# Performance work log

Hardware: AMD Instinct MI355X
Metric: run time of the kernel (lower is better)

## Reference

```python
import jax, jax.numpy as jnp
import numpy as np

B, N = 2, 2048
DIM, NH, DH = 640, 10, 64
DINNER = 2560
L = 4
DEMB = 32
NTOKS = [128, 64]
NFEAT = 19
FDIM = 280
FEATD = DIM - DEMB * len(NTOKS)  # 576
SQRTD = float(np.sqrt(DH))


def _ln(x, g, b, eps=1e-5):
    m = jnp.mean(x, -1, keepdims=True)
    v = jnp.var(x, -1, keepdims=True)
    return (x - m) * jax.lax.rsqrt(v + eps) * g + b


def setup_inputs() -> dict:
    key = jax.random.key(0)
    ks = iter(jax.random.split(key, 32))
    s = 0.05
    return {
        "x_feats": jax.random.normal(next(ks), (B, N, NFEAT), jnp.float32),
        "x_toks": jax.random.randint(next(ks), (B, N, 2), 0, 64),
        "mask": jnp.ones((B, N), jnp.float32),
        "emb0": jax.random.normal(next(ks), (NTOKS[0] + 1, DEMB)) * s,
        "emb1": jax.random.normal(next(ks), (NTOKS[1] + 1, DEMB)) * s,
        "feat_w": jax.random.normal(next(ks), (FEATD, NFEAT)) * s,
        "feat_b": jnp.zeros((FEATD,)),
        "qkv_w": jax.random.normal(next(ks), (L, 3 * DIM, DIM)) * s,
        "qkv_b": jnp.zeros((L, 3 * DIM)),
        "o_w": jax.random.normal(next(ks), (L, DIM, DIM)) * s,
        "ln1_g": jnp.ones((L, DIM)), "ln1_b": jnp.zeros((L, DIM)),
        "ln2_g": jnp.ones((L, DIM)), "ln2_b": jnp.zeros((L, DIM)),
        "p1_w": jax.random.normal(next(ks), (L, DINNER, DIM)) * s,
        "p1_b": jnp.zeros((L, DINNER)),
        "p2_w": jax.random.normal(next(ks), (L, DIM, DINNER)) * s,
        "p2_b": jnp.zeros((L, DIM)),
        "fn_g": jnp.ones((DIM,)), "fn_b": jnp.zeros((DIM,)),
        "lin1_w": jax.random.normal(next(ks), (FDIM, DIM)) * s,
        "lin1_b": jnp.zeros((FDIM,)),
        "rb1_w": jax.random.normal(next(ks), (FDIM, FDIM)) * s,
        "rb1_b": jnp.zeros((FDIM,)),
        "rb2_w": jax.random.normal(next(ks), (FDIM, FDIM)) * s,
        "rb2_b": jnp.zeros((FDIM,)),
        "out_w": jax.random.normal(next(ks), (1, FDIM)) * s,
        "out_b": jnp.zeros((1,)),
    }


def _forward(x_feats, x_toks, mask, emb0, emb1, feat_w, feat_b,
             qkv_w, qkv_b, o_w, ln1_g, ln1_b, ln2_g, ln2_b,
             p1_w, p1_b, p2_w, p2_b, fn_g, fn_b,
             lin1_w, lin1_b, rb1_w, rb1_b, rb2_w, rb2_b, out_w, out_b):
    # mask outer product [B,N,N]; additive mask 0 where allowed, -1e20 elsewhere
    mask2 = jnp.einsum('bi,bj->bij', mask, mask)
    add_mask = jnp.where(mask2 > 0, 0.0, -1e20)

    # embeddings + feature projection -> [B,N,DIM]
    Z = jnp.concatenate([emb0[x_toks[..., 0]], emb1[x_toks[..., 1]],
                         x_feats @ feat_w.T + feat_b], axis=-1)

    def layer(Z, prm):
        qw, qb, ow, g1, b1, g2, b2, w1, c1, w2, c2 = prm
        inp = Z
        Zn = _ln(Z, g1, b1)
        # qkv reshaped to [B,N,H,3*DH], chunked along last dim: V, Q, K
        qkv = (Zn @ qw.T + qb).reshape(B, N, NH, 3 * DH)
        V, Q, K = qkv[..., :DH], qkv[..., DH:2 * DH], qkv[..., 2 * DH:]
        W = jnp.einsum('bnhd,bmhd->bhnm', Q, K) / SQRTD + add_mask[:, None]
        W = jax.nn.softmax(W, axis=3) * mask2[:, None]  # post-softmax mult mask
        attn = jnp.einsum('bhnm,bmhd->bnhd', W, V).reshape(B, N, DIM)
        Z = jax.nn.leaky_relu(attn) @ ow.T + inp  # leaky_relu BEFORE o_net
        inp = Z
        Zn = _ln(Z, g2, b2)
        Z = jax.nn.relu(Zn @ w1.T + c1) @ w2.T + c2 + inp
        return Z, None

    Z, _ = jax.lax.scan(layer, Z,
                        (qkv_w, qkv_b, o_w, ln1_g, ln1_b, ln2_g, ln2_b,
                         p1_w, p1_b, p2_w, p2_b))
    Z = _ln(Z, fn_g, fn_b)
    # ranking head: 1x1 convs == per-token linears
    h = Z @ lin1_w.T + lin1_b
    h = h + (jax.nn.relu(h @ rb1_w.T + rb1_b) @ rb2_w.T + rb2_b)
    return (h @ out_w.T + out_b)[..., 0]  # [B,N]


def reference(x_feats, x_toks, mask, emb0, emb1, feat_w, feat_b,
              qkv_w, qkv_b, o_w, ln1_g, ln1_b, ln2_g, ln2_b,
              p1_w, p1_b, p2_w, p2_b, fn_g, fn_b,
              lin1_w, lin1_b, rb1_w, rb1_b, rb2_w, rb2_b, out_w, out_b):
    return _forward(x_feats, x_toks, mask, emb0, emb1, feat_w, feat_b,
                    qkv_w, qkv_b, o_w, ln1_g, ln1_b, ln2_g, ln2_b,
                    p1_w, p1_b, p2_w, p2_b, fn_g, fn_b,
                    lin1_w, lin1_b, rb1_w, rb1_b, rb2_w, rb2_b, out_w, out_b)
```

## Files before the change

### kernel.cpp

```cpp
#include <hip/hip_runtime.h>

#define B_ 2
#define N_ 2048
#define DIM_ 640
#define NH_ 10
#define DH_ 64
#define DINNER_ 2560
#define L_ 4
#define FDIM_ 280
#define FDIMP_ 320
#define FEATD_ 576
#define NFEAT_ 19
#define ROWS_ (B_*N_)

typedef __attribute__((ext_vector_type(8))) unsigned short ushort8;
typedef __attribute__((ext_vector_type(8))) __bf16 bf16x8;
typedef __attribute__((ext_vector_type(4))) __bf16 bf16x4;
typedef __attribute__((ext_vector_type(4))) float f32x4;
typedef __attribute__((ext_vector_type(2))) unsigned int u32x2;

static __device__ __forceinline__ unsigned short f2bf(float f){
  unsigned int u = __builtin_bit_cast(unsigned int, f);
  u += 0x7fffu + ((u >> 16) & 1u);
  return (unsigned short)(u >> 16);
}

static __device__ __forceinline__ f32x4 mfma16(ushort8 a, ushort8 b, f32x4 c){
  return __builtin_amdgcn_mfma_f32_16x16x32_bf16(
      __builtin_bit_cast(bf16x8, a), __builtin_bit_cast(bf16x8, b), c, 0, 0, 0);
}

#define GLD(src,dst) __builtin_amdgcn_global_load_lds((const __attribute__((address_space(1))) void*)(src), (__attribute__((address_space(3))) void*)(dst), 16, 0, 0)

#define SEG0 4915200
#define SEG1 1638400
#define SEG2 6553600
#define SEG3 6553600
#define SEG4 179200
#define SEG5 89600
#define SEG6 89600
#define SEG7 655360
#define SEG8 655360
#define SEG9 4096
#define E0 SEG0
#define E1 (E0+SEG1)
#define E2 (E1+SEG2)
#define E3 (E2+SEG3)
#define E4 (E3+SEG4)
#define E5 (E4+SEG5)
#define E6 (E5+SEG6)
#define E7 (E6+SEG7)
#define E8 (E7+SEG8)
#define E9 (E8+SEG9)

__global__ __launch_bounds__(256) void prep_kernel(
    const float* __restrict__ qkv_w, const float* __restrict__ o_w,
    const float* __restrict__ p1_w, const float* __restrict__ p2_w,
    const float* __restrict__ lin1_w, const float* __restrict__ rb1_w,
    const float* __restrict__ rb2_w, const float* __restrict__ mask,
    unsigned short* __restrict__ qkvw, unsigned short* __restrict__ oww,
    unsigned short* __restrict__ p1w, unsigned short* __restrict__ p2w,
    unsigned short* __restrict__ l1w, unsigned short* __restrict__ r1w,
    unsigned short* __restrict__ r2w, unsigned int* __restrict__ hb1z,
    unsigned int* __restrict__ hb2z, float* __restrict__ mbb)
{
  for (int i = blockIdx.x*256 + threadIdx.x; i < E9; i += gridDim.x*256){
    int j = i;
    if (j < E0) { qkvw[j] = f2bf(qkv_w[j]); continue; }
    j -= E0;
    if (j < SEG1) { oww[j] = f2bf(o_w[j]); continue; }
    j -= SEG1;
    if (j < SEG2) { p1w[j] = f2bf(p1_w[j]); continue; }
    j -= SEG2;
    if (j < SEG3) { p2w[j] = f2bf(p2_w[j]); continue; }
    j -= SEG3;
    if (j < SEG4) { l1w[j] = f2bf(lin1_w[j]); continue; }
    j -= SEG4;
    if (j < SEG5) { int r = j/FDIMP_, c = j - r*FDIMP_;
                    r1w[j] = (c<FDIM_) ? f2bf(rb1_w[r*FDIM_+c]) : (unsigned short)0; continue; }
    j -= SEG5;
    if (j < SEG6) { int r = j/FDIMP_, c = j - r*FDIMP_;
                    r2w[j] = (c<FDIM_) ? f2bf(rb2_w[r*FDIM_+c]) : (unsigned short)0; continue; }
    j -= SEG6;
    if (j < SEG7) { hb1z[j] = 0u; continue; }
    j -= SEG7;
    if (j < SEG8) { hb2z[j] = 0u; continue; }
    j -= SEG8;
    mbb[j] = (mask[j] > 0.f) ? 0.f : -1e30f;
  }
}

__global__ __launch_bounds__(256) void embed_kernel(const float* __restrict__ xf,
    const int* __restrict__ xt, const float* __restrict__ e0, const float* __restrict__ e1,
    const float* __restrict__ fw, const float* __restrict__ fb, float* __restrict__ Z){
  int row = blockIdx.x;
  __shared__ float f[NFEAT_];
  int t = threadIdx.x;
  if (t < NFEAT_) f[t] = xf[row*NFEAT_ + t];
  __syncthreads();
  if (t < 32) {
    int tok0 = xt[row*2];
    Z[(size_t)row*DIM_ + t] = e0[tok0*32 + t];
  } else if (t < 64) {
    int tok1 = xt[row*2+1];
    Z[(size_t)row*DIM_ + t] = e1[tok1*32 + (t-32)];
  }
  for (int fo = t; fo < FEATD_; fo += 256){
    float acc = fb[fo];
    #pragma unroll
    for (int k=0;k<NFEAT_;k++) acc += f[k]*fw[fo*NFEAT_+k];
    Z[(size_t)row*DIM_ + 64 + fo] = acc;
  }
}

__global__ __launch_bounds__(256) void ln_kernel(const float* __restrict__ X,
    const float* __restrict__ g, const float* __restrict__ bb,
    unsigned short* __restrict__ out){
  int lane = threadIdx.x & 63;
  int row = blockIdx.x*4 + (threadIdx.x >> 6);
  const float* x = X + (size_t)row*DIM_;
  float v[10]; float s=0.f, sq=0.f;
  #pragma unroll
  for (int j=0;j<10;j++){ float t = x[lane + j*64]; v[j]=t; s+=t; sq+=t*t; }
  #pragma unroll
  for (int off=1; off<64; off<<=1){ s += __shfl_xor(s, off, 64); sq += __shfl_xor(sq, off, 64); }
  float mean = s*(1.f/DIM_);
  float var = sq*(1.f/DIM_) - mean*mean;
  float rstd = rsqrtf(var + 1e-5f);
  unsigned short* o = out + (size_t)row*DIM_;
  #pragma unroll
  for (int j=0;j<10;j++){ int c = lane + j*64; o[c] = f2bf((v[j]-mean)*rstd*g[c] + bb[c]); }
}

template<bool BIAS, bool RELU, bool RES, bool OUTF, bool OUTB>
__global__ __launch_bounds__(256) void gemm_kernel(
    const unsigned short* __restrict__ A, int lda,
    const unsigned short* __restrict__ Bw, int ldb,
    const float* __restrict__ bias,
    const float* __restrict__ Res, int ldres,
    float* __restrict__ Cf, int ldcf,
    unsigned short* __restrict__ Cb, int ldcb,
    int Ncols, int K)
{
  __shared__ __align__(16) unsigned short As[3][128*32];
  __shared__ __align__(16) unsigned short Bs[3][128*32];
  int t = threadIdx.x;
  int wid = t >> 6, lane = t & 63;
  int wr = wid >> 1, wc = wid & 1;
  int lg = lane >> 4, lm = lane & 15;
  int row0 = blockIdx.y * 128;
  int col0 = blockIdx.x * 128;

  int c0 = wid*128 + lane, c1 = c0 + 64;
  int ar0 = c0 >> 2, aq0 = c0 & 3;
  int ar1 = c1 >> 2, aq1 = c1 & 3;
  const unsigned short* a0 = A + (size_t)(row0+ar0)*lda + aq0*8;
  const unsigned short* a1 = A + (size_t)(row0+ar1)*lda + aq1*8;
  int br0 = col0+ar0; if (br0 >= Ncols) br0 = Ncols-1;
  int br1 = col0+ar1; if (br1 >= Ncols) br1 = Ncols-1;
  const unsigned short* b0 = Bw + (size_t)br0*ldb + aq0*8;
  const unsigned short* b1 = Bw + (size_t)br1*ldb + aq1*8;

  f32x4 acc[4][4];
  #pragma unroll
  for (int m=0;m<4;m++)
    #pragma unroll
    for (int n=0;n<4;n++) acc[m][n] = f32x4{0.f,0.f,0.f,0.f};

  int nk = K >> 5;
  GLD(a0, &As[0][c0*8]); GLD(b0, &Bs[0][c0*8]);
  GLD(a1, &As[0][c1*8]); GLD(b1, &Bs[0][c1*8]);
  if (nk > 1){
    GLD(a0+32, &As[1][c0*8]); GLD(b0+32, &Bs[1][c0*8]);
    GLD(a1+32, &As[1][c1*8]); GLD(b1+32, &Bs[1][c1*8]);
  }

  int cur = 0;
  for (int tk=0; tk<nk; ++tk){
    if (tk+2 < nk){
      int st = (cur >= 1) ? cur-1 : 2;
      int koff = (tk+2) << 5;
      GLD(a0+koff, &As[st][c0*8]); GLD(b0+koff, &Bs[st][c0*8]);
      GLD(a1+koff, &As[st][c1*8]); GLD(b1+koff, &Bs[st][c1*8]);
    }
    int rem = nk-1-tk;
    if (rem > 1)       asm volatile("s_waitcnt vmcnt(8)" ::: "memory");
    else if (rem == 1) asm volatile("s_waitcnt vmcnt(4)" ::: "memory");
    else               asm volatile("s_waitcnt vmcnt(0)" ::: "memory");
    __builtin_amdgcn_s_barrier();
    asm volatile("" ::: "memory");
    const unsigned short* Ac = &As[cur][0];
    const unsigned short* Bc = &Bs[cur][0];
    ushort8 af[4], bfr[4];
    #pragma unroll
    for (int m=0;m<4;m++) af[m] = *(const ushort8*)(Ac + (wr*64 + m*16 + lm)*32 + lg*8);
    #pragma unroll
    for (int n=0;n<4;n++) bfr[n] = *(const ushort8*)(Bc + (wc*64 + n*16 + lm)*32 + lg*8);
    #pragma unroll
    for (int m=0;m<4;m++)
      #pragma unroll
      for (int n=0;n<4;n++)
        acc[m][n] = mfma16(af[m], bfr[n], acc[m][n]);
    asm volatile("" ::: "memory");
    __builtin_amdgcn_s_barrier();
    cur = (cur == 2) ? 0 : cur+1;
  }

  #pragma unroll
  for (int m=0;m<4;m++){
    int rbase = row0 + wr*64 + m*16 + lg*4;
    #pragma unroll
    for (int n=0;n<4;n++){
      int cc = col0 + wc*64 + n*16 + lm;
      if (cc < Ncols){
        float bv = 0.f;
        if (BIAS) bv = bias[cc];
        #pragma unroll
        for (int rr=0;rr<4;rr++){
          float v = acc[m][n][rr] + bv;
          if (RELU) v = fmaxf(v, 0.f);
          if (RES) v += Res[(size_t)(rbase+rr)*ldres + cc];
          if (OUTF) Cf[(size_t)(rbase+rr)*ldcf + cc] = v;
          if (OUTB) Cb[(size_t)(rbase+rr)*ldcb + cc] = f2bf(v);
        }
      }
    }
  }
}

template<bool BIAS, bool RELU, bool RES, bool OUTF, bool OUTB>
__global__ __launch_bounds__(256) void gemm64_kernel(
    const unsigned short* __restrict__ A, int lda,
    const unsigned short* __restrict__ Bw, int ldb,
    const float* __restrict__ bias,
    const float* __restrict__ Res, int ldres,
    float* __restrict__ Cf, int ldcf,
    unsigned short* __restrict__ Cb, int ldcb,
    int Ncols, int K)
{
  __shared__ __align__(16) unsigned short As[3][64*64];
  __shared__ __align__(16) unsigned short Bs[3][64*64];
  int t = threadIdx.x;
  int wid = t >> 6, lane = t & 63;
  int wr = wid >> 1, wc = wid & 1;
  int lg = lane >> 4, lm = lane & 15;
  int row0 = blockIdx.y * 64;
  int col0 = blockIdx.x * 64;

  int ar0 = t >> 3, aq = t & 7;
  int ar1 = ar0 + 32;
  const unsigned short* a0 = A + (size_t)(row0+ar0)*lda + aq*8;
  const unsigned short* a1 = A + (size_t)(row0+ar1)*lda + aq*8;
  int br0 = col0+ar0; if (br0 >= Ncols) br0 = Ncols-1;
  int br1 = col0+ar1; if (br1 >= Ncols) br1 = Ncols-1;
  const unsigned short* b0 = Bw + (size_t)br0*ldb + aq*8;
  const unsigned short* b1 = Bw + (size_t)br1*ldb + aq*8;
  int l0 = ar0*64 + aq*8, l1 = ar1*64 + aq*8;

  f32x4 acc[2][2];
  #pragma unroll
  for (int m=0;m<2;m++)
    #pragma unroll
    for (int n=0;n<2;n++) acc[m][n] = f32x4{0.f,0.f,0.f,0.f};

  int nk = K >> 6;
  GLD(a0, &As[0][l0]); GLD(b0, &Bs[0][l0]);
  GLD(a1, &As[0][l1]); GLD(b1, &Bs[0][l1]);
  if (nk > 1){
    GLD(a0+64, &As[1][l0]); GLD(b0+64, &Bs[1][l0]);
    GLD(a1+64, &As[1][l1]); GLD(b1+64, &Bs[1][l1]);
  }

  int cur = 0;
  for (int tk=0; tk<nk; ++tk){
    if (tk+2 < nk){
      int st = (cur >= 1) ? cur-1 : 2;
      int koff = (tk+2) << 6;
      GLD(a0+koff, &As[st][l0]); GLD(b0+koff, &Bs[st][l0]);
      GLD(a1+koff, &As[st][l1]); GLD(b1+koff, &Bs[st][l1]);
    }
    int rem = nk-1-tk;
    if (rem > 1)       asm volatile("s_waitcnt vmcnt(8)" ::: "memory");
    else if (rem == 1) asm volatile("s_waitcnt vmcnt(4)" ::: "memory");
    else               asm volatile("s_waitcnt vmcnt(0)" ::: "memory");
    __builtin_amdgcn_s_barrier();
    asm volatile("" ::: "memory");
    const unsigned short* Ac = &As[cur][0];
    const unsigned short* Bc = &Bs[cur][0];
    ushort8 af[2][2], bfr[2][2];
    #pragma unroll
    for (int kk=0;kk<2;kk++){
      #pragma unroll
      for (int m=0;m<2;m++) af[kk][m] = *(const ushort8*)(Ac + (wr*32 + m*16 + lm)*64 + kk*32 + lg*8);
      #pragma unroll
      for (int n=0;n<2;n++) bfr[kk][n] = *(const ushort8*)(Bc + (wc*32 + n*16 + lm)*64 + kk*32 + lg*8);
    }
    #pragma unroll
    for (int kk=0;kk<2;kk++)
      #pragma unroll
      for (int m=0;m<2;m++)
        #pragma unroll
        for (int n=0;n<2;n++)
          acc[m][n] = mfma16(af[kk][m], bfr[kk][n], acc[m][n]);
    asm volatile("" ::: "memory");
    __builtin_amdgcn_s_barrier();
    cur = (cur == 2) ? 0 : cur+1;
  }

  #pragma unroll
  for (int m=0;m<2;m++){
    int rbase = row0 + wr*32 + m*16 + lg*4;
    #pragma unroll
    for (int n=0;n<2;n++){
      int cc = col0 + wc*32 + n*16 + lm;
      if (cc < Ncols){
        float bv = 0.f;
        if (BIAS) bv = bias[cc];
        #pragma unroll
        for (int rr=0;rr<4;rr++){
          float v = acc[m][n][rr] + bv;
          if (RELU) v = fmaxf(v, 0.f);
          if (RES) v += Res[(size_t)(rbase+rr)*ldres + cc];
          if (OUTF) Cf[(size_t)(rbase+rr)*ldcf + cc] = v;
          if (OUTB) Cb[(size_t)(rbase+rr)*ldcb + cc] = f2bf(v);
        }
      }
    }
  }
}

__global__ __launch_bounds__(256) void attn_kernel(const unsigned short* __restrict__ qkv,
    const float* __restrict__ mb, unsigned short* __restrict__ att){
  int bh = blockIdx.y; int b = bh/NH_, h = bh%NH_;
  int t = threadIdx.x; int wid = t>>6, lane = t&63, lg = lane>>4, lm = lane&15;
  int q0 = blockIdx.x*64 + wid*16;

  __shared__ __align__(128) unsigned short Ks[2][4096];
  __shared__ __align__(128) unsigned short Vs[2][4096];
  __shared__ __align__(16) float maskL[N_];

  const size_t base = (size_t)b*N_*1920 + (size_t)h*192;

  int c0 = t, c1 = t+256;
  int kk0 = c0>>3, kc0 = (c0&7)^(kk0&7);
  int kk1 = c1>>3, kc1 = (c1&7)^(kk1&7);
  const unsigned short* kS0 = qkv + base + 128 + (size_t)kk0*1920 + kc0*8;
  const unsigned short* kS1 = qkv + base + 128 + (size_t)kk1*1920 + kc1*8;
  int vk0 = ((c0>>5)<<2)|((c0>>1)&3), vd0 = (((c0>>3)&3)<<1)|(c0&1);
  int vk1 = ((c1>>5)<<2)|((c1>>1)&3), vd1 = (((c1>>3)&3)<<1)|(c1&1);
  const unsigned short* vS0 = qkv + base + (size_t)vk0*1920 + vd0*8;
  const unsigned short* vS1 = qkv + base + (size_t)vk1*1920 + vd1*8;

  ushort8 qf[2];
  #pragma unroll
  for (int ss=0; ss<2; ss++)
    qf[ss] = *(const ushort8*)(qkv + base + (size_t)(q0+lm)*1920 + 64 + ss*32 + lg*8);
  float cb2 = mb[b*N_ + q0 + lm] - 17.3123405f;

  GLD(mb + b*N_ + c0*4, &maskL[c0*4]);
  GLD(mb + b*N_ + c1*4, &maskL[c1*4]);
  GLD(kS0, &Ks[0][c0*8]); GLD(kS1, &Ks[0][c1*8]);
  GLD(vS0, &Vs[0][c0*8]); GLD(vS1, &Vs[0][c1*8]);

  float lp = 0.f;
  f32x4 o[4];
  #pragma unroll
  for (int dn=0;dn<4;dn++) o[dn] = f32x4{0.f,0.f,0.f,0.f};

  for (int it=0; it<N_/64; ++it){
    int cur = it & 1;
    if (it < N_/64 - 1){
      const size_t adv = (size_t)(it+1)*64*1920;
      GLD(kS0+adv, &Ks[1-cur][c0*8]); GLD(kS1+adv, &Ks[1-cur][c1*8]);
      GLD(vS0+adv, &Vs[1-cur][c0*8]); GLD(vS1+adv, &Vs[1-cur][c1*8]);
      asm volatile("s_waitcnt vmcnt(4)" ::: "memory");
    } else {
      asm volatile("s_waitcnt vmcnt(0)" ::: "memory");
    }
    __builtin_amdgcn_s_barrier();
    asm volatile("" ::: "memory");

    const unsigned short* Kc = &Ks[cur][0];
    f32x4 sf[4];
    #pragma unroll
    for (int c=0;c<4;c++){
      int krow = c*16 + lm;
      f32x4 s = f32x4{0.f,0.f,0.f,0.f};
      #pragma unroll
      for (int ss=0;ss<2;ss++){
        ushort8 kf = *(const ushort8*)(Kc + (krow*8 + ((ss*4+lg)^(krow&7)))*8);
        s = mfma16(kf, qf[ss], s);
      }
      sf[c] = s;
    }
    f32x4 mkv[4];
    #pragma unroll
    for (int c=0;c<4;c++) mkv[c] = *(const f32x4*)&maskL[it*64 + c*16 + lg*4];

    unsigned vsb = (unsigned)(size_t)(__attribute__((address_space(3))) unsigned short*)&Vs[cur][0];
    unsigned a0 = vsb + lg*512 + lm*8;
    u32x2 vb[4][4];
    asm volatile(
      "ds_read_b64_tr_b16 %0, %4 offset:0\n\t"
      "ds_read_b64_tr_b16 %1, %4 offset:128\n\t"
      "ds_read_b64_tr_b16 %2, %4 offset:256\n\t"
      "ds_read_b64_tr_b16 %3, %4 offset:384"
      : "=&v"(vb[0][0]),"=&v"(vb[0][1]),"=&v"(vb[0][2]),"=&v"(vb[0][3]) : "v"(a0));
    asm volatile(
      "ds_read_b64_tr_b16 %0, %4 offset:2048\n\t"
      "ds_read_b64_tr_b16 %1, %4 offset:2176\n\t"
      "ds_read_b64_tr_b16 %2, %4 offset:2304\n\t"
      "ds_read_b64_tr_b16 %3, %4 offset:2432"
      : "=&v"(vb[1][0]),"=&v"(vb[1][1]),"=&v"(vb[1][2]),"=&v"(vb[1][3]) : "v"(a0));
    asm volatile(
      "ds_read_b64_tr_b16 %0, %4 offset:4096\n\t"
      "ds_read_b64_tr_b16 %1, %4 offset:4224\n\t"
      "ds_read_b64_tr_b16 %2, %4 offset:4352\n\t"
      "ds_read_b64_tr_b16 %3, %4 offset:4480"
      : "=&v"(vb[2][0]),"=&v"(vb[2][1]),"=&v"(vb[2][2]),"=&v"(vb[2][3]) : "v"(a0));
    asm volatile(
      "ds_read_b64_tr_b16 %0, %4 offset:6144\n\t"
      "ds_read_b64_tr_b16 %1, %4 offset:6272\n\t"
      "ds_read_b64_tr_b16 %2, %4 offset:6400\n\t"
      "ds_read_b64_tr_b16 %3, %4 offset:6528"
      : "=&v"(vb[3][0]),"=&v"(vb[3][1]),"=&v"(vb[3][2]),"=&v"(vb[3][3]) : "v"(a0));

    float pm[4][4]; bf16x4 pa[4];
    #pragma unroll
    for (int c=0;c<4;c++){
      #pragma unroll
      for (int r=0;r<4;r++){
        float x = fmaf(sf[c][r], 0.18033688f, cb2 + mkv[c][r]);
        pm[c][r] = exp2f(x);
      }
      lp += (pm[c][0]+pm[c][1]) + (pm[c][2]+pm[c][3]);
      pa[c] = bf16x4{(__bf16)pm[c][0], (__bf16)pm[c][1], (__bf16)pm[c][2], (__bf16)pm[c][3]};
    }

#define PVM(dn_, c_) asm("v_mfma_f32_16x16x16_bf16 %0, %1, %2, %0" \
      : "+v"(o[dn_]) : "v"(__builtin_bit_cast(u32x2, pa[c_])), "v"(vb[c_][dn_]))
    asm volatile("s_waitcnt lgkmcnt(8)" ::: "memory");
    __builtin_amdgcn_sched_barrier(0);
    __builtin_amdgcn_s_setprio(1);
    PVM(0,0); PVM(1,0); PVM(2,0); PVM(3,0);
    PVM(0,1); PVM(1,1); PVM(2,1); PVM(3,1);
    asm volatile("s_waitcnt lgkmcnt(0)" ::: "memory");
    __builtin_amdgcn_sched_barrier(0);
    PVM(0,2); PVM(1,2); PVM(2,2); PVM(3,2);
    PVM(0,3); PVM(1,3); PVM(2,3); PVM(3,3);
    __builtin_amdgcn_s_setprio(0);
#undef PVM
    asm volatile("" ::: "memory");
    __builtin_amdgcn_s_barrier();
  }

  float s = lp;
  s += __shfl_xor(s, 16, 64);
  s += __shfl_xor(s, 32, 64);
  float inv = 1.0f / fmaxf(s, 1e-30f);
  #pragma unroll
  for (int r=0;r<4;r++){
    float ir = __shfl(inv, (lane & 48) | (lg*4 + r), 64);
    #pragma unroll
    for (int dn=0;dn<4;dn++){
      float v = o[dn][r] * ir;
      v = (v >= 0.f) ? v : 0.01f*v;
      att[(size_t)(b*N_ + q0 + lg*4 + r)*DIM_ + h*64 + dn*16 + lm] = f2bf(v);
    }
  }
}

__global__ __launch_bounds__(256) void out_kernel(const float* __restrict__ hf,
    const float* __restrict__ ow, const float* __restrict__ ob, float* __restrict__ out){
  int lane = threadIdx.x & 63;
  int row = blockIdx.x*4 + (threadIdx.x>>6);
  const float* x = hf + (size_t)row*FDIM_;
  float s = 0.f;
  for (int j=lane;j<FDIM_;j+=64) s += x[j]*ow[j];
  #pragma unroll
  for (int off=1; off<64; off<<=1) s += __shfl_xor(s, off, 64);
  if (lane==0) out[row] = s + ob[0];
}

extern "C" void kernel_launch(void* const* d_in, const int* in_sizes, int n_in,
                              void* d_out, int out_size, void* d_ws, size_t ws_size,
                              hipStream_t stream)
{
  const float* x_feats = (const float*)d_in[0];
  const int*   x_toks  = (const int*)d_in[1];
  const float* mask    = (const float*)d_in[2];
  const float* emb0    = (const float*)d_in[3];
  const float* emb1    = (const float*)d_in[4];
  const float* feat_w  = (const float*)d_in[5];
  const float* feat_b  = (const float*)d_in[6];
  const float* qkv_w   = (const float*)d_in[7];
  const float* qkv_b   = (const float*)d_in[8];
  const float* o_w     = (const float*)d_in[9];
  const float* ln1_g   = (const float*)d_in[10];
  const float* ln1_b   = (const float*)d_in[11];
  const float* ln2_g   = (const float*)d_in[12];
  const float* ln2_b   = (const float*)d_in[13];
  const float* p1_w    = (const float*)d_in[14];
  const float* p1_b    = (const float*)d_in[15];
  const float* p2_w    = (const float*)d_in[16];
  const float* p2_b    = (const float*)d_in[17];
  const float* fn_g    = (const float*)d_in[18];
  const float* fn_b    = (const float*)d_in[19];
  const float* lin1_w  = (const float*)d_in[20];
  const float* lin1_b  = (const float*)d_in[21];
  const float* rb1_w   = (const float*)d_in[22];
  const float* rb1_b   = (const float*)d_in[23];
  const float* rb2_w   = (const float*)d_in[24];
  const float* rb2_b   = (const float*)d_in[25];
  const float* out_w   = (const float*)d_in[26];
  const float* out_b   = (const float*)d_in[27];
  float* out = (float*)d_out;

  char* w = (char*)d_ws;
  auto alloc = [&](size_t bytes)->void*{ void* p = (void*)w; w += (bytes + 255) & ~(size_t)255; return p; };

  float* Z              = (float*)alloc((size_t)ROWS_*DIM_*4);
  unsigned short* Zn    = (unsigned short*)alloc((size_t)ROWS_*DIM_*2);
  unsigned short* qkvB  = (unsigned short*)alloc((size_t)ROWS_*1920*2);
  unsigned short* attB  = (unsigned short*)alloc((size_t)ROWS_*DIM_*2);
  unsigned short* Hb    = (unsigned short*)alloc((size_t)ROWS_*DINNER_*2);
  float* hf             = (float*)alloc((size_t)ROWS_*FDIM_*4);
  unsigned short* hb1   = (unsigned short*)alloc((size_t)ROWS_*FDIMP_*2);
  unsigned short* hb2   = (unsigned short*)alloc((size_t)ROWS_*FDIMP_*2);
  float* mbb            = (float*)alloc((size_t)ROWS_*4);
  unsigned short* qkvw  = (unsigned short*)alloc((size_t)L_*1920*DIM_*2);
  unsigned short* oww   = (unsigned short*)alloc((size_t)L_*DIM_*DIM_*2);
  unsigned short* p1w   = (unsigned short*)alloc((size_t)L_*DINNER_*DIM_*2);
  unsigned short* p2w   = (unsigned short*)alloc((size_t)L_*DIM_*DINNER_*2);
  unsigned short* l1w   = (unsigned short*)alloc((size_t)FDIM_*DIM_*2);
  unsigned short* r1w   = (unsigned short*)alloc((size_t)FDIM_*FDIMP_*2);
  unsigned short* r2w   = (unsigned short*)alloc((size_t)FDIM_*FDIMP_*2);

  prep_kernel<<<2048,256,0,stream>>>(qkv_w, o_w, p1_w, p2_w, lin1_w, rb1_w, rb2_w, mask,
      qkvw, oww, p1w, p2w, l1w, r1w, r2w,
      (unsigned int*)hb1, (unsigned int*)hb2, mbb);

  embed_kernel<<<ROWS_,256,0,stream>>>(x_feats, x_toks, emb0, emb1, feat_w, feat_b, Z);

  for (int l=0; l<L_; l++){
    ln_kernel<<<ROWS_/4,256,0,stream>>>(Z, ln1_g + l*DIM_, ln1_b + l*DIM_, Zn);
    gemm_kernel<true,false,false,false,true><<<dim3(15,32),256,0,stream>>>(
        Zn, DIM_, qkvw + (size_t)l*1920*DIM_, DIM_, qkv_b + l*1920,
        nullptr, 0, nullptr, 0, qkvB, 1920, 1920, DIM_);
    attn_kernel<<<dim3(N_/64, B_*NH_),256,0,stream>>>(qkvB, mbb, attB);
    gemm64_kernel<false,false,true,true,false><<<dim3(10,64),256,0,stream>>>(
        attB, DIM_, oww + (size_t)l*DIM_*DIM_, DIM_, nullptr,
        Z, DIM_, Z, DIM_, nullptr, 0, DIM_, DIM_);
    ln_kernel<<<ROWS_/4,256,0,stream>>>(Z, ln2_g + l*DIM_, ln2_b + l*DIM_, Zn);
    gemm_kernel<true,true,false,false,true><<<dim3(20,32),256,0,stream>>>(
        Zn, DIM_, p1w + (size_t)l*DINNER_*DIM_, DIM_, p1_b + l*DINNER_,
        nullptr, 0, nullptr, 0, Hb, DINNER_, DINNER_, DIM_);
    gemm64_kernel<true,false,true,true,false><<<dim3(10,64),256,0,stream>>>(
        Hb, DINNER_, p2w + (size_t)l*DIM_*DINNER_, DINNER_, p2_b + l*DIM_,
        Z, DIM_, Z, DIM_, nullptr, 0, DIM_, DINNER_);
  }

  ln_kernel<<<ROWS_/4,256,0,stream>>>(Z, fn_g, fn_b, Zn);
  gemm64_kernel<true,false,false,true,true><<<dim3(5,64),256,0,stream>>>(
      Zn, DIM_, l1w, DIM_, lin1_b, nullptr, 0, hf, FDIM_, hb1, FDIMP_, FDIM_, DIM_);
  gemm64_kernel<true,true,false,false,true><<<dim3(5,64),256,0,stream>>>(
      hb1, FDIMP_, r1w, FDIMP_, rb1_b, nullptr, 0, nullptr, 0, hb2, FDIMP_, FDIM_, FDIMP_);
  gemm64_kernel<true,false,true,true,false><<<dim3(5,64),256,0,stream>>>(
      hb2, FDIMP_, r2w, FDIMP_, rb2_b, hf, FDIM_, hf, FDIM_, nullptr, 0, FDIM_, FDIMP_);
  out_kernel<<<ROWS_/4,256,0,stream>>>(hf, out_w, out_b, out);
}
```

Baseline: 757.4 us.

## Split attention over key dimension into two partial blocks with reduction kernel

Result: faster. 715.1 us (-5.6%).

```diff
diff --git a/kernel.cpp b/kernel.cpp
--- a/kernel.cpp
+++ b/kernel.cpp
@@ -12,8 +12,10 @@
 #define FEATD_ 576
 #define NFEAT_ 19
 #define ROWS_ (B_*N_)
+#define NITS_ 16
 
 typedef __attribute__((ext_vector_type(8))) unsigned short ushort8;
+typedef __attribute__((ext_vector_type(4))) unsigned short ushort4v;
 typedef __attribute__((ext_vector_type(8))) __bf16 bf16x8;
 typedef __attribute__((ext_vector_type(4))) __bf16 bf16x4;
 typedef __attribute__((ext_vector_type(4))) float f32x4;
@@ -330,26 +332,29 @@
 }
 
 __global__ __launch_bounds__(256) void attn_kernel(const unsigned short* __restrict__ qkv,
-    const float* __restrict__ mb, unsigned short* __restrict__ att){
+    const float* __restrict__ mb, float* __restrict__ op, float* __restrict__ lpp){
   int bh = blockIdx.y; int b = bh/NH_, h = bh%NH_;
   int t = threadIdx.x; int wid = t>>6, lane = t&63, lg = lane>>4, lm = lane&15;
   int q0 = blockIdx.x*64 + wid*16;
+  int it0 = blockIdx.z * NITS_;
+  size_t prow = (size_t)blockIdx.z*ROWS_ + b*N_;
 
   __shared__ __align__(128) unsigned short Ks[2][4096];
   __shared__ __align__(128) unsigned short Vs[2][4096];
-  __shared__ __align__(16) float maskL[N_];
+  __shared__ __align__(16) float maskL[NITS_*64];
 
   const size_t base = (size_t)b*N_*1920 + (size_t)h*192;
+  const size_t kvoff = (size_t)it0*64*1920;
 
   int c0 = t, c1 = t+256;
   int kk0 = c0>>3, kc0 = (c0&7)^(kk0&7);
   int kk1 = c1>>3, kc1 = (c1&7)^(kk1&7);
-  const unsigned short* kS0 = qkv + base + 128 + (size_t)kk0*1920 + kc0*8;
-  const unsigned short* kS1 = qkv + base + 128 + (size_t)kk1*1920 + kc1*8;
+  const unsigned short* kS0 = qkv + base + kvoff + 128 + (size_t)kk0*1920 + kc0*8;
+  const unsigned short* kS1 = qkv + base + kvoff + 128 + (size_t)kk1*1920 + kc1*8;
   int vk0 = ((c0>>5)<<2)|((c0>>1)&3), vd0 = (((c0>>3)&3)<<1)|(c0&1);
   int vk1 = ((c1>>5)<<2)|((c1>>1)&3), vd1 = (((c1>>3)&3)<<1)|(c1&1);
-  const unsigned short* vS0 = qkv + base + (size_t)vk0*1920 + vd0*8;
-  const unsigned short* vS1 = qkv + base + (size_t)vk1*1920 + vd1*8;
+  const unsigned short* vS0 = qkv + base + kvoff + (size_t)vk0*1920 + vd0*8;
+  const unsigned short* vS1 = qkv + base + kvoff + (size_t)vk1*1920 + vd1*8;
 
   ushort8 qf[2];
   #pragma unroll
@@ -357,8 +362,7 @@
     qf[ss] = *(const ushort8*)(qkv + base + (size_t)(q0+lm)*1920 + 64 + ss*32 + lg*8);
   float cb2 = mb[b*N_ + q0 + lm] - 17.3123405f;
 
-  GLD(mb + b*N_ + c0*4, &maskL[c0*4]);
-  GLD(mb + b*N_ + c1*4, &maskL[c1*4]);
+  GLD(mb + b*N_ + it0*64 + t*4, &maskL[t*4]);
   GLD(kS0, &Ks[0][c0*8]); GLD(kS1, &Ks[0][c1*8]);
   GLD(vS0, &Vs[0][c0*8]); GLD(vS1, &Vs[0][c1*8]);
 
@@ -367,10 +371,10 @@
   #pragma unroll
   for (int dn=0;dn<4;dn++) o[dn] = f32x4{0.f,0.f,0.f,0.f};
 
-  for (int it=0; it<N_/64; ++it){
-    int cur = it & 1;
-    if (it < N_/64 - 1){
-      const size_t adv = (size_t)(it+1)*64*1920;
+  for (int ii=0; ii<NITS_; ++ii){
+    int cur = ii & 1;
+    if (ii < NITS_ - 1){
+      const size_t adv = (size_t)(ii+1)*64*1920;
       GLD(kS0+adv, &Ks[1-cur][c0*8]); GLD(kS1+adv, &Ks[1-cur][c1*8]);
       GLD(vS0+adv, &Vs[1-cur][c0*8]); GLD(vS1+adv, &Vs[1-cur][c1*8]);
       asm volatile("s_waitcnt vmcnt(4)" ::: "memory");
@@ -395,7 +399,7 @@
     }
     f32x4 mkv[4];
     #pragma unroll
-    for (int c=0;c<4;c++) mkv[c] = *(const f32x4*)&maskL[it*64 + c*16 + lg*4];
+    for (int c=0;c<4;c++) mkv[c] = *(const f32x4*)&maskL[ii*64 + c*16 + lg*4];
 
     unsigned vsb = (unsigned)(size_t)(__attribute__((address_space(3))) unsigned short*)&Vs[cur][0];
     unsigned a0 = vsb + lg*512 + lm*8;
@@ -431,7 +435,7 @@
       #pragma unroll
       for (int r=0;r<4;r++){
         float x = fmaf(sf[c][r], 0.18033688f, cb2 + mkv[c][r]);
-        pm[c][r] = exp2f(x);
+        pm[c][r] = __builtin_amdgcn_exp2f(x);
       }
       lp += (pm[c][0]+pm[c][1]) + (pm[c][2]+pm[c][3]);
       pa[c] = bf16x4{(__bf16)pm[c][0], (__bf16)pm[c][1], (__bf16)pm[c][2], (__bf16)pm[c][3]};
@@ -457,17 +461,34 @@
   float s = lp;
   s += __shfl_xor(s, 16, 64);
   s += __shfl_xor(s, 32, 64);
-  float inv = 1.0f / fmaxf(s, 1e-30f);
+  if (lg == 0) lpp[(prow + q0 + lm)*NH_ + h] = s;
   #pragma unroll
   for (int r=0;r<4;r++){
-    float ir = __shfl(inv, (lane & 48) | (lg*4 + r), 64);
-    #pragma unroll
-    for (int dn=0;dn<4;dn++){
-      float v = o[dn][r] * ir;
-      v = (v >= 0.f) ? v : 0.01f*v;
-      att[(size_t)(b*N_ + q0 + lg*4 + r)*DIM_ + h*64 + dn*16 + lm] = f2bf(v);
-    }
-  }
+    float* ob = op + (prow + q0 + lg*4 + r)*DIM_ + h*64;
+    #pragma unroll
+    for (int dn=0;dn<4;dn++)
+      ob[dn*16 + lm] = o[dn][r];
+  }
+}
+
+__global__ __launch_bounds__(256) void attnred_kernel(const float* __restrict__ op,
+    const float* __restrict__ lpp, unsigned short* __restrict__ att){
+  int idx = blockIdx.x*256 + threadIdx.x;
+  int row = idx / 160;
+  int c4 = (idx - row*160) * 4;
+  int h = c4 >> 6;
+  f32x4 o0 = *(const f32x4*)(op + (size_t)row*DIM_ + c4);
+  f32x4 o1 = *(const f32x4*)(op + ((size_t)ROWS_ + row)*DIM_ + c4);
+  float l = lpp[row*NH_ + h] + lpp[(ROWS_ + row)*NH_ + h];
+  float inv = 1.0f / fmaxf(l, 1e-30f);
+  ushort4v rr;
+  #pragma unroll
+  for (int j=0;j<4;j++){
+    float v = (o0[j] + o1[j]) * inv;
+    v = (v >= 0.f) ? v : 0.01f*v;
+    rr[j] = f2bf(v);
+  }
+  *(ushort4v*)(att + (size_t)row*DIM_ + c4) = rr;
 }
 
 __global__ __launch_bounds__(256) void out_kernel(const float* __restrict__ hf,
@@ -528,6 +549,8 @@
   unsigned short* hb1   = (unsigned short*)alloc((size_t)ROWS_*FDIMP_*2);
   unsigned short* hb2   = (unsigned short*)alloc((size_t)ROWS_*FDIMP_*2);
   float* mbb            = (float*)alloc((size_t)ROWS_*4);
+  float* opart          = (float*)alloc((size_t)2*ROWS_*DIM_*4);
+  float* lpart          = (float*)alloc((size_t)2*ROWS_*NH_*4);
   unsigned short* qkvw  = (unsigned short*)alloc((size_t)L_*1920*DIM_*2);
   unsigned short* oww   = (unsigned short*)alloc((size_t)L_*DIM_*DIM_*2);
   unsigned short* p1w   = (unsigned short*)alloc((size_t)L_*DINNER_*DIM_*2);
@@ -547,7 +570,8 @@
     gemm_kernel<true,false,false,false,true><<<dim3(15,32),256,0,stream>>>(
         Zn, DIM_, qkvw + (size_t)l*1920*DIM_, DIM_, qkv_b + l*1920,
         nullptr, 0, nullptr, 0, qkvB, 1920, 1920, DIM_);
-    attn_kernel<<<dim3(N_/64, B_*NH_),256,0,stream>>>(qkvB, mbb, attB);
+    attn_kernel<<<dim3(N_/64, B_*NH_, 2),256,0,stream>>>(qkvB, mbb, opart, lpart);
+    attnred_kernel<<<ROWS_*160/256,256,0,stream>>>(opart, lpart, attB);
     gemm64_kernel<false,false,true,true,false><<<dim3(10,64),256,0,stream>>>(
         attB, DIM_, oww + (size_t)l*DIM_*DIM_, DIM_, nullptr,
         Z, DIM_, Z, DIM_, nullptr, 0, DIM_, DIM_);
```
